# Optimization experiments

Hardware: AMD Instinct MI355X
Metric: run time of the kernel (lower is better)

The kernel has to match this reference:

```python
import jax, jax.numpy as jnp
import numpy as np

B = 2; NPB = 65536; N = B * NPB      # voxels, equal count per batch (divisible by group size)
C = 128; H = 4; DH = C // H          # model dim, heads, head dim
GS = 4096; T = 64                    # window group size, retention chunk length
SPARSE = (32, 468, 468)              # sparse_shape (z, y, x)
WIN = (13, 13, 32)                   # window_shape (x, y, z)


def _mappings(coords):
    # get_window_coors_shift_v2 (shift=False) + x/y Hilbert-like in-window orders, then sort.
    sz, sy, sx = SPARSE
    wx, wy, wz = WIN
    mx = int(np.ceil(sx / wx) + 1); my = int(np.ceil(sy / wy) + 1); mz = int(np.ceil(sz / wz) + 1)
    per = mx * my * mz
    b = coords[:, 0]; z = coords[:, 1]; y = coords[:, 2]; x = coords[:, 3]
    wcx, wcy, wcz = x // wx, y // wy, z // wz
    cx, cy, cz = x % wx, y % wy, z % wz
    bwx = b * per + wcx * (my * mz) + wcy * mz + wcz
    bwy = b * per + wcy * (mx * mz) + wcx * mz + wcz
    wvol = wx * wy * wz
    vx = bwx * wvol + cx * (wy * wz) + cy * wz + cz
    vy = bwy * wvol + cy * (wx * wz) + cx * wz + cz
    return jnp.argsort(vx), jnp.argsort(vy)


def _retnet_block(x, Wq, Wk, Wv, Wg, Wo):
    # x: [G, L, C]; per-head decayed linear attention (RetNet), chunked recurrent form.
    G, L, _ = x.shape
    nch = L // T
    gamma = 1.0 - jnp.exp2(-5.0 - jnp.arange(H, dtype=x.dtype))  # [H]

    def heads(w):
        return (x @ w).reshape(G, L, H, DH).transpose(0, 2, 1, 3)  # [G,H,L,dh]

    q = heads(Wq) * (DH ** -0.5); k = heads(Wk); v = heads(Wv)

    def chunks(t):
        return t.reshape(G, H, nch, T, DH).transpose(2, 0, 1, 3, 4)  # [nch,G,H,T,dh]

    qc, kc, vc = chunks(q), chunks(k), chunks(v)
    i = jnp.arange(T)
    expo = i[:, None] - i[None, :]
    D = jnp.where(expo >= 0, gamma[:, None, None] ** jnp.maximum(expo, 0), 0.0)  # [H,T,T] causal decay
    cross_d = gamma[:, None] ** (i + 1)[None, :]        # [H,T] state->token decay
    kv_d = gamma[:, None] ** (T - 1 - i)[None, :]       # [H,T] token->state decay
    chunk_d = gamma ** T

    def step(S, qkv):  # S: [G,H,dh,dh]
        qt, kt, vt = qkv
        attn = jnp.einsum('ghtd,ghsd->ghts', qt, kt) * D[None]
        inner = jnp.einsum('ghts,ghsd->ghtd', attn, vt)
        cross = jnp.einsum('ghtd,ghde->ghte', qt * cross_d[None, :, :, None], S)
        S = chunk_d[None, :, None, None] * S + jnp.einsum('ghtd,ghte->ghde', kt * kv_d[None, :, :, None], vt)
        return S, inner + cross

    S0 = jnp.zeros((G, H, DH, DH), x.dtype)
    _, ys = jax.lax.scan(step, S0, (qc, kc, vc))  # [nch,G,H,T,dh]
    y = ys.transpose(1, 2, 0, 3, 4).reshape(G, H, L, DH).transpose(0, 2, 1, 3).reshape(G, L, C)
    return x + (y * jax.nn.silu(x @ Wg)) @ Wo


def setup_inputs():
    key = jax.random.key(0)
    ks = jax.random.split(key, 16)
    feats = jax.random.normal(ks[0], (N, C), jnp.float32)
    b = jnp.repeat(jnp.arange(B, dtype=jnp.int32), NPB)
    z = jax.random.randint(ks[1], (N,), 0, SPARSE[0], dtype=jnp.int32)
    y = jax.random.randint(ks[2], (N,), 0, SPARSE[1], dtype=jnp.int32)
    x = jax.random.randint(ks[3], (N,), 0, SPARSE[2], dtype=jnp.int32)
    coords = jnp.stack([b, z, y, x], axis=1)
    w = lambda k: jax.random.normal(k, (C, C), jnp.float32) * (C ** -0.5)
    names = ['Wq0', 'Wk0', 'Wv0', 'Wg0', 'Wo0', 'Wq1', 'Wk1', 'Wv1', 'Wg1', 'Wo1']
    d = {'feats': feats, 'coords': coords}
    for n_, k_ in zip(names, ks[4:14]):
        d[n_] = w(k_)
    return d


def reference(feats, coords, Wq0, Wk0, Wv0, Wg0, Wo0, Wq1, Wk1, Wv1, Wg1, Wo1):
    # Per-batch counts are equal and divisible by GS, so flat2win/win2flat are identity maps.
    ix, iy = _mappings(coords)
    f = feats
    for idx, W in ((ix, (Wq0, Wk0, Wv0, Wg0, Wo0)), (iy, (Wq1, Wk1, Wv1, Wg1, Wo1))):
        xf = f[idx].reshape(-1, GS, C)     # gather sorted windows
        xf = _retnet_block(xf, *W)         # per-window linear RNN
        f = f.at[idx].set(xf.reshape(-1, C))  # scatter back
    return f
```

## Files before the change

### kernel.cpp

```cpp
#include <hip/hip_runtime.h>
#include <hip/hip_bf16.h>

#define NPTS 131072
#define CF   128
#define GS   4096
#define PER  2738
#define NBKT 5476
#define NCHUNK 2048

typedef short v8s __attribute__((ext_vector_type(8)));
typedef float v4f __attribute__((ext_vector_type(4)));
#define MFMA16(a,b,c) __builtin_amdgcn_mfma_f32_16x16x32_bf16(a,b,c,0,0,0)

__device__ __forceinline__ unsigned short f2b(float x) {
    unsigned u = __float_as_uint(x);
    unsigned r = (u + 0x7FFFu + ((u >> 16) & 1u)) >> 16;
    return (unsigned short)r;
}
__device__ __forceinline__ unsigned pack2(float a, float b) {
    return (unsigned)f2b(a) | ((unsigned)f2b(b) << 16);
}
__device__ __forceinline__ float b2f(unsigned short s) {
    return __uint_as_float((unsigned)s << 16);
}

__global__ void k_zero(int* a, int* b, int* c, int* d) {
    int t = blockIdx.x * 256 + threadIdx.x;
    if (t < 8192) { a[t] = 0; b[t] = 0; c[t] = 0; d[t] = 0; }
}

__global__ void k_keys(const int* __restrict__ coords, int* cntx, int* cnty) {
    int j = blockIdx.x * 256 + threadIdx.x;
    if (j >= NPTS) return;
    int b = coords[4*j], z = coords[4*j+1], y = coords[4*j+2], x = coords[4*j+3];
    int wcx = x / 13, wcy = y / 13, wcz = z / 32;
    atomicAdd(&cntx[b * PER + wcx * 74 + wcy * 2 + wcz], 1);
    atomicAdd(&cnty[b * PER + wcy * 74 + wcx * 2 + wcz], 1);
}

__global__ __launch_bounds__(256) void k_bscan(const int* __restrict__ cntx, int* offx,
                                               const int* __restrict__ cnty, int* offy) {
    const int* cnt = blockIdx.x ? cnty : cntx;
    int* off = blockIdx.x ? offy : offx;
    __shared__ int part[256];
    int t = threadIdx.x;
    const int CH = (NBKT + 255) / 256;
    int s = 0;
    for (int i = 0; i < CH; i++) { int idx = t * CH + i; if (idx < NBKT) s += cnt[idx]; }
    part[t] = s;
    __syncthreads();
    for (int d = 1; d < 256; d <<= 1) {
        int v = (t >= d) ? part[t - d] : 0;
        __syncthreads();
        part[t] += v;
        __syncthreads();
    }
    int base = (t == 0) ? 0 : part[t - 1];
    for (int i = 0; i < CH; i++) {
        int idx = t * CH + i;
        if (idx < NBKT) { off[idx] = base; base += cnt[idx]; }
    }
}

__global__ void k_scatter(const int* __restrict__ coords,
                          const int* __restrict__ offx, int* curx, int* bkx,
                          const int* __restrict__ offy, int* cury, int* bky) {
    int j = blockIdx.x * 256 + threadIdx.x;
    if (j >= NPTS) return;
    int b = coords[4*j], z = coords[4*j+1], y = coords[4*j+2], x = coords[4*j+3];
    int wcx = x / 13, wcy = y / 13, wcz = z / 32;
    int cx = x - wcx * 13, cy = y - wcy * 13, cz = z - wcz * 32;
    int px = offx[b*PER + wcx*74 + wcy*2 + wcz] + atomicAdd(&curx[b*PER + wcx*74 + wcy*2 + wcz], 1);
    bkx[px] = ((cx * 416 + cy * 32 + cz) << 17) | j;
    int py = offy[b*PER + wcy*74 + wcx*2 + wcz] + atomicAdd(&cury[b*PER + wcy*74 + wcx*2 + wcz], 1);
    bky[py] = ((cy * 416 + cx * 32 + cz) << 17) | j;
}

__global__ __launch_bounds__(256) void k_bsort(const int* offx, const int* cntx, const int* bkx, int* ix,
                                               const int* offy, const int* cnty, const int* bky, int* iy) {
    const int* off; const int* cnt; const int* bk; int* oidx;
    if (blockIdx.y == 0) { off = offx; cnt = cntx; bk = bkx; oidx = ix; }
    else                 { off = offy; cnt = cnty; bk = bky; oidx = iy; }
    int b = blockIdx.x;
    int n = cnt[b];
    if (n <= 0) return;
    int base = off[b];
    __shared__ int keys[256];
    int t = threadIdx.x;
    if (t < n) keys[t] = bk[base + t];
    __syncthreads();
    if (t < n) {
        int kv = keys[t];
        int r = 0;
        for (int j = 0; j < n; j++) r += (keys[j] < kv);
        oidx[base + r] = kv & 0x1FFFF;
    }
}

struct WP { const float* p[10]; };
__global__ void k_cvtw(WP wp, unsigned short* __restrict__ WT) {
    int i = blockIdx.x * 256 + threadIdx.x;
    int w = i >> 14, r = i & 16383, c = r >> 7, d = r & 127;
    float v = wp.p[w][c * 128 + d];
    if (w == 0 || w == 5) v *= 0.17677669529663687f;
    WT[(size_t)w * 16384 + d * 128 + c] = f2b(v);
}

__global__ __launch_bounds__(256) void k_qkvA(const float* __restrict__ src,
        const int* __restrict__ idx,
        const unsigned short* __restrict__ WTq, const unsigned short* __restrict__ WTk,
        const unsigned short* __restrict__ WTv,
        unsigned short* __restrict__ qb, unsigned short* __restrict__ kb,
        unsigned short* __restrict__ vtb, float* __restrict__ At) {
    __shared__ unsigned short kt[128 * 72];
    __shared__ unsigned short vt[128 * 72];
    const int chunk = blockIdx.x;
    const int t = threadIdx.x, w = t >> 6, lane = t & 63, l15 = lane & 15, kg = lane >> 4;
    const int rtok = chunk * 64 + w * 16 + l15;
    const int srow = idx[rtok];
    const int sloc = w * 16 + l15;
    float w63[4];
#pragma unroll
    for (int h = 0; h < 4; h++) {
        float l2g = log2f(1.f - exp2f(-5.f - (float)h));
        w63[h] = exp2f((float)(63 - sloc) * l2g);
    }
    v8s xf[4];
    const float* xr = src + (size_t)srow * 128;
#pragma unroll
    for (int ks = 0; ks < 4; ks++) {
        int c0 = ks * 32 + kg * 8;
        float4 a = *(const float4*)(xr + c0);
        float4 b = *(const float4*)(xr + c0 + 4);
        v8s v;
        v[0]=(short)f2b(a.x); v[1]=(short)f2b(a.y); v[2]=(short)f2b(a.z); v[3]=(short)f2b(a.w);
        v[4]=(short)f2b(b.x); v[5]=(short)f2b(b.y); v[6]=(short)f2b(b.z); v[7]=(short)f2b(b.w);
        xf[ks] = v;
    }
#pragma unroll
    for (int dt = 0; dt < 8; dt++) {
        v4f acc = {0.f, 0.f, 0.f, 0.f};
#pragma unroll
        for (int ks = 0; ks < 4; ks++) {
            v8s wf = *(const v8s*)(WTq + (size_t)(dt * 16 + l15) * 128 + ks * 32 + kg * 8);
            acc = MFMA16(wf, xf[ks], acc);
        }
        int2 p; p.x = pack2(acc[0], acc[1]); p.y = pack2(acc[2], acc[3]);
        *(int2*)(qb + (size_t)rtok * 128 + dt * 16 + kg * 4) = p;
    }
#pragma unroll
    for (int dt = 0; dt < 8; dt++) {
        v4f acc = {0.f, 0.f, 0.f, 0.f};
#pragma unroll
        for (int ks = 0; ks < 4; ks++) {
            v8s wf = *(const v8s*)(WTk + (size_t)(dt * 16 + l15) * 128 + ks * 32 + kg * 8);
            acc = MFMA16(wf, xf[ks], acc);
        }
        int2 p; p.x = pack2(acc[0], acc[1]); p.y = pack2(acc[2], acc[3]);
        *(int2*)(kb + (size_t)rtok * 128 + dt * 16 + kg * 4) = p;
        float dec = w63[dt >> 1];
        int d0 = dt * 16 + kg * 4;
#pragma unroll
        for (int j = 0; j < 4; j++) kt[(d0 + j) * 72 + sloc] = f2b(acc[j] * dec);
    }
#pragma unroll
    for (int et = 0; et < 8; et++) {
        v4f acc = {0.f, 0.f, 0.f, 0.f};
#pragma unroll
        for (int ks = 0; ks < 4; ks++) {
            v8s wf = *(const v8s*)(WTv + (size_t)(et * 16 + l15) * 128 + ks * 32 + kg * 8);
            acc = MFMA16(xf[ks], wf, acc);
        }
        int e_glob = et * 16 + l15, h = e_glob >> 5, e = e_glob & 31, s0 = w * 16 + kg * 4;
        int2 p; p.x = pack2(acc[0], acc[1]); p.y = pack2(acc[2], acc[3]);
        *(int2*)(vtb + ((size_t)(chunk * 4 + h) * 2048) + e * 64 + s0) = p;
        *(int2*)(vt + e_glob * 72 + s0) = p;
    }
    __syncthreads();
    {
        int h = w, g = chunk >> 6, c = chunk & 63;
        size_t base = ((size_t)(g * 4 + h) * 64 + c) * 1024;
#pragma unroll
        for (int dt2 = 0; dt2 < 2; dt2++)
#pragma unroll
        for (int et2 = 0; et2 < 2; et2++) {
            v4f acc = {0.f, 0.f, 0.f, 0.f};
#pragma unroll
            for (int ks2 = 0; ks2 < 2; ks2++) {
                v8s af = *(const v8s*)(kt + (h * 32 + dt2 * 16 + l15) * 72 + ks2 * 32 + kg * 8);
                v8s bf = *(const v8s*)(vt + (h * 32 + et2 * 16 + l15) * 72 + ks2 * 32 + kg * 8);
                acc = MFMA16(af, bf, acc);
            }
            *(v4f*)(At + base + (et2 * 16 + l15) * 32 + dt2 * 16 + kg * 4) = acc;
        }
    }
}

__global__ __launch_bounds__(256) void k_sscan(const float* __restrict__ At,
                                               unsigned short* __restrict__ Sbt) {
    int b = blockIdx.x, gh = b >> 2, q = b & 3, h = gh & 3;
    int p = q * 256 + threadIdx.x;
    float gT = exp2f(64.f * log2f(1.f - exp2f(-5.f - (float)h)));
    size_t base = (size_t)gh * 64 * 1024 + p;
    float s = 0.f;
#pragma unroll 4
    for (int c = 0; c < 64; c++) {
        float a = At[base + (size_t)c * 1024];
        Sbt[base + (size_t)c * 1024] = f2b(s);
        s = gT * s + a;
    }
}

__global__ __launch_bounds__(256) void k_attnf(const float* __restrict__ src,
        const int* __restrict__ idx,
        const unsigned short* __restrict__ qb, const unsigned short* __restrict__ kb,
        const unsigned short* __restrict__ vtb, const unsigned short* __restrict__ Sbt,
        const unsigned short* __restrict__ WTg, const unsigned short* __restrict__ WTo,
        float* __restrict__ outp) {
    __shared__ float gp[4][144];
    __shared__ unsigned short Pl[64 * 104];
    __shared__ unsigned short VTl[32 * 104];
    __shared__ unsigned short Zl[64 * 136];
    const int chunk = blockIdx.x;
    const int t = threadIdx.x, w = t >> 6, lane = t & 63, l15 = lane & 15, kg = lane >> 4;
    const int rl = w * 16 + l15;
    const int rtok = chunk * 64 + rl;
    const int srow = idx[rtok];
    {
        float l2gv[4];
#pragma unroll
        for (int h = 0; h < 4; h++) l2gv[h] = log2f(1.f - exp2f(-5.f - (float)h));
        for (int i = t; i < 576; i += 256) {
            int h = i / 144, m = i - h * 144;
            gp[h][m] = exp2f((float)(m - 64) * l2gv[h]);
        }
    }
    v4f yacc[8];
#pragma unroll
    for (int i = 0; i < 8; i++) yacc[i] = (v4f){0.f, 0.f, 0.f, 0.f};

    const size_t sb_base = ((size_t)((chunk >> 6) * 4) * 64 + (chunk & 63)) * 1024;
#pragma unroll
    for (int h = 0; h < 4; h++) {
        __syncthreads();
        {
            int e = t >> 3, s0 = (t & 7) * 8;
            v8s vv = *(const v8s*)(vtb + (size_t)(chunk * 4 + h) * 2048 + e * 64 + s0);
            *(v8s*)(VTl + e * 104 + s0) = vv;
            if (t < 128) {
                int e2 = t >> 2, d0 = (t & 3) * 8;
                v8s sv = *(const v8s*)(Sbt + sb_base + (size_t)h * 64 * 1024 + e2 * 32 + d0);
                *(v8s*)(VTl + e2 * 104 + 64 + d0) = sv;
            }
        }
        __syncthreads();
        v8s qf = *(const v8s*)(qb + (size_t)rtok * 128 + h * 32 + kg * 8);
        v4f Tf[4];
#pragma unroll
        for (int st = 0; st < 4; st++) {
            v8s kf = *(const v8s*)(kb + (size_t)(chunk * 64 + st * 16 + l15) * 128 + h * 32 + kg * 8);
            Tf[st] = MFMA16(kf, qf, ((v4f){0.f, 0.f, 0.f, 0.f}));
        }
        float gi1 = gp[h][63], gi2 = gp[h][62], gi3 = gp[h][61];
#pragma unroll
        for (int st = 0; st < 4; st++) {
            int s0 = st * 16 + kg * 4;
            float g0 = gp[h][64 + rl - s0];
            float v0 = (rl >= s0    ) ? Tf[st][0] * g0       : 0.f;
            float v1 = (rl >= s0 + 1) ? Tf[st][1] * g0 * gi1 : 0.f;
            float v2 = (rl >= s0 + 2) ? Tf[st][2] * g0 * gi2 : 0.f;
            float v3 = (rl >= s0 + 3) ? Tf[st][3] * g0 * gi3 : 0.f;
            int2 p; p.x = pack2(v0, v1); p.y = pack2(v2, v3);
            *(int2*)(Pl + rl * 104 + s0) = p;
        }
        {
            float gc = gp[h][65 + rl];
            float q0 = b2f((unsigned short)qf[0]) * gc, q1 = b2f((unsigned short)qf[1]) * gc;
            float q2 = b2f((unsigned short)qf[2]) * gc, q3 = b2f((unsigned short)qf[3]) * gc;
            float q4 = b2f((unsigned short)qf[4]) * gc, q5 = b2f((unsigned short)qf[5]) * gc;
            float q6 = b2f((unsigned short)qf[6]) * gc, q7 = b2f((unsigned short)qf[7]) * gc;
            int2 pa; pa.x = pack2(q0, q1); pa.y = pack2(q2, q3);
            *(int2*)(Pl + rl * 104 + 64 + kg * 8) = pa;
            int2 pb; pb.x = pack2(q4, q5); pb.y = pack2(q6, q7);
            *(int2*)(Pl + rl * 104 + 64 + kg * 8 + 4) = pb;
        }
#pragma unroll
        for (int et = 0; et < 2; et++) {
            v4f acc = yacc[h * 2 + et];
#pragma unroll
            for (int ks = 0; ks < 3; ks++) {
                v8s vf = *(const v8s*)(VTl + (et * 16 + l15) * 104 + ks * 32 + kg * 8);
                v8s pf = *(const v8s*)(Pl + rl * 104 + ks * 32 + kg * 8);
                acc = MFMA16(vf, pf, acc);
            }
            yacc[h * 2 + et] = acc;
        }
    }
    v8s xg[4];
    {
        const float* xr = src + (size_t)srow * 128;
#pragma unroll
        for (int ks = 0; ks < 4; ks++) {
            int c0 = ks * 32 + kg * 8;
            float4 a = *(const float4*)(xr + c0);
            float4 b = *(const float4*)(xr + c0 + 4);
            v8s v;
            v[0]=(short)f2b(a.x); v[1]=(short)f2b(a.y); v[2]=(short)f2b(a.z); v[3]=(short)f2b(a.w);
            v[4]=(short)f2b(b.x); v[5]=(short)f2b(b.y); v[6]=(short)f2b(b.z); v[7]=(short)f2b(b.w);
            xg[ks] = v;
        }
    }
#pragma unroll
    for (int ct = 0; ct < 8; ct++) {
        v4f g = {0.f, 0.f, 0.f, 0.f};
#pragma unroll
        for (int ks = 0; ks < 4; ks++) {
            v8s wf = *(const v8s*)(WTg + (size_t)(ct * 16 + l15) * 128 + ks * 32 + kg * 8);
            g = MFMA16(wf, xg[ks], g);
        }
        v4f yv = yacc[ct];
        float z0 = yv[0] * (g[0] / (1.f + __expf(-g[0])));
        float z1 = yv[1] * (g[1] / (1.f + __expf(-g[1])));
        float z2 = yv[2] * (g[2] / (1.f + __expf(-g[2])));
        float z3 = yv[3] * (g[3] / (1.f + __expf(-g[3])));
        int2 p; p.x = pack2(z0, z1); p.y = pack2(z2, z3);
        *(int2*)(Zl + rl * 136 + ct * 16 + kg * 4) = p;
    }
    v8s zf[4];
#pragma unroll
    for (int ks = 0; ks < 4; ks++)
        zf[ks] = *(const v8s*)(Zl + rl * 136 + ks * 32 + kg * 8);
    const float* xr = src + (size_t)srow * 128;
#pragma unroll
    for (int cot = 0; cot < 8; cot++) {
        v4f acc = {0.f, 0.f, 0.f, 0.f};
#pragma unroll
        for (int ks = 0; ks < 4; ks++) {
            v8s wf = *(const v8s*)(WTo + (size_t)(cot * 16 + l15) * 128 + ks * 32 + kg * 8);
            acc = MFMA16(wf, zf[ks], acc);
        }
        int c0 = cot * 16 + kg * 4;
        float4 xres = *(const float4*)(xr + c0);
        float4 o;
        o.x = xres.x + acc[0]; o.y = xres.y + acc[1];
        o.z = xres.z + acc[2]; o.w = xres.w + acc[3];
        *(float4*)(outp + (size_t)srow * 128 + c0) = o;
    }
}

static void run_pass(const float* src, const int* idx, const unsigned short* WT, int wbase,
                     unsigned short* qb, unsigned short* kb, unsigned short* vtb,
                     float* At, unsigned short* Sbt, float* out, hipStream_t stream) {
    k_qkvA<<<NCHUNK, 256, 0, stream>>>(src, idx, WT + (size_t)(wbase+0)*16384,
                                       WT + (size_t)(wbase+1)*16384, WT + (size_t)(wbase+2)*16384,
                                       qb, kb, vtb, At);
    k_sscan<<<512, 256, 0, stream>>>(At, Sbt);
    k_attnf<<<NCHUNK, 256, 0, stream>>>(src, idx, qb, kb, vtb, Sbt,
                                        WT + (size_t)(wbase+3)*16384, WT + (size_t)(wbase+4)*16384, out);
}

extern "C" void kernel_launch(void* const* d_in, const int* in_sizes, int n_in,
                              void* d_out, int out_size, void* d_ws, size_t ws_size,
                              hipStream_t stream) {
    const float* feats  = (const float*)d_in[0];
    const int*   coords = (const int*)d_in[1];
    float* out = (float*)d_out;

    char* wptr = (char*)d_ws;
    unsigned short* qb  = (unsigned short*)wptr; wptr += (size_t)NPTS * 128 * 2;
    unsigned short* kb  = (unsigned short*)wptr; wptr += (size_t)NPTS * 128 * 2;
    unsigned short* vtb = (unsigned short*)wptr; wptr += (size_t)NPTS * 128 * 2;
    float* At           = (float*)wptr;          wptr += (size_t)NCHUNK * 4096 * 4;
    unsigned short* Sbt = (unsigned short*)wptr; wptr += (size_t)NCHUNK * 4096 * 2;
    unsigned short* WT  = (unsigned short*)wptr; wptr += (size_t)10 * 16384 * 2;
    int* ix   = (int*)wptr; wptr += (size_t)NPTS * 4;
    int* iy   = (int*)wptr; wptr += (size_t)NPTS * 4;
    int* bkx  = (int*)wptr; wptr += (size_t)NPTS * 4;
    int* bky  = (int*)wptr; wptr += (size_t)NPTS * 4;
    int* cntx = (int*)wptr; wptr += 8192 * 4;
    int* cnty = (int*)wptr; wptr += 8192 * 4;
    int* offx = (int*)wptr; wptr += 8192 * 4;
    int* offy = (int*)wptr; wptr += 8192 * 4;
    int* curx = (int*)wptr; wptr += 8192 * 4;
    int* cury = (int*)wptr; wptr += 8192 * 4;

    WP wp;
    for (int i = 0; i < 10; i++) wp.p[i] = (const float*)d_in[2 + i];
    k_cvtw<<<640, 256, 0, stream>>>(wp, WT);

    k_zero<<<32, 256, 0, stream>>>(cntx, cnty, curx, cury);
    k_keys<<<(NPTS + 255) / 256, 256, 0, stream>>>(coords, cntx, cnty);
    k_bscan<<<2, 256, 0, stream>>>(cntx, offx, cnty, offy);
    k_scatter<<<(NPTS + 255) / 256, 256, 0, stream>>>(coords, offx, curx, bkx, offy, cury, bky);
    k_bsort<<<dim3(NBKT, 2), 256, 0, stream>>>(offx, cntx, bkx, ix, offy, cnty, bky, iy);

    run_pass(feats, ix, WT, 0, qb, kb, vtb, At, Sbt, out, stream);
    run_pass(out,   iy, WT, 5, qb, kb, vtb, At, Sbt, out, stream);
}
```

Baseline: 648.3 us.

## Split chunk-state kernel, store decayed K, and replace LDS staging with cross-lane shuffles

The QKV kernel now stages the gathered input rows through shared memory with coalesced loads, and it stores K already scaled by its in-chunk decay. Computing the chunk K^T V state moves into a separate kernel that reads K and V back from global memory. The attention kernel drops its shared-memory buffers and barriers: decay factors are computed in closed form and the P/Z operand layouts are rebuilt with wave shuffles. The state scan preloads all 64 chunk values into registers. This trades an extra launch and extra global traffic for fewer LDS round trips and syncs.

```diff
diff --git a/kernel.cpp b/kernel.cpp
--- a/kernel.cpp
+++ b/kernel.cpp
@@ -2,8 +2,6 @@
 #include <hip/hip_bf16.h>
 
 #define NPTS 131072
-#define CF   128
-#define GS   4096
 #define PER  2738
 #define NBKT 5476
 #define NCHUNK 2048
@@ -22,6 +20,23 @@
 }
 __device__ __forceinline__ float b2f(unsigned short s) {
     return __uint_as_float((unsigned)s << 16);
+}
+
+__device__ __forceinline__ v8s redist(int2 a, int2 b, int lane) {
+    int l15 = lane & 15, kg = lane >> 4;
+    int m0 = l15 + 16 * ((2 * kg) & 3);
+    int m1 = l15 + 16 * ((2 * kg + 1) & 3);
+    int ax0 = __shfl(a.x, m0, 64), ay0 = __shfl(a.y, m0, 64);
+    int ax1 = __shfl(a.x, m1, 64), ay1 = __shfl(a.y, m1, 64);
+    int bx0 = __shfl(b.x, m0, 64), by0 = __shfl(b.y, m0, 64);
+    int bx1 = __shfl(b.x, m1, 64), by1 = __shfl(b.y, m1, 64);
+    bool hi = kg >= 2;
+    union { int i[4]; v8s v; } u;
+    u.i[0] = hi ? bx0 : ax0;
+    u.i[1] = hi ? by0 : ay0;
+    u.i[2] = hi ? bx1 : ax1;
+    u.i[3] = hi ? by1 : ay1;
+    return u.v;
 }
 
 __global__ void k_zero(int* a, int* b, int* c, int* d) {
@@ -106,37 +121,37 @@
     WT[(size_t)w * 16384 + d * 128 + c] = f2b(v);
 }
 
-__global__ __launch_bounds__(256) void k_qkvA(const float* __restrict__ src,
+__global__ __launch_bounds__(256) void k_qkv(const float* __restrict__ src,
         const int* __restrict__ idx,
         const unsigned short* __restrict__ WTq, const unsigned short* __restrict__ WTk,
         const unsigned short* __restrict__ WTv,
-        unsigned short* __restrict__ qb, unsigned short* __restrict__ kb,
-        unsigned short* __restrict__ vtb, float* __restrict__ At) {
-    __shared__ unsigned short kt[128 * 72];
-    __shared__ unsigned short vt[128 * 72];
+        unsigned short* __restrict__ qb, unsigned short* __restrict__ kbh,
+        unsigned short* __restrict__ vtb) {
+    __shared__ unsigned short Xl[64 * 136];
     const int chunk = blockIdx.x;
     const int t = threadIdx.x, w = t >> 6, lane = t & 63, l15 = lane & 15, kg = lane >> 4;
-    const int rtok = chunk * 64 + w * 16 + l15;
-    const int srow = idx[rtok];
+#pragma unroll
+    for (int i = 0; i < 8; i++) {
+        int r = i * 8 + (t >> 5);
+        int col = (t & 31) * 4;
+        int srow = idx[chunk * 64 + r];
+        float4 v = *(const float4*)(src + (size_t)srow * 128 + col);
+        uint2 p; p.x = pack2(v.x, v.y); p.y = pack2(v.z, v.w);
+        *(uint2*)(Xl + r * 136 + col) = p;
+    }
+    __syncthreads();
     const int sloc = w * 16 + l15;
+    const int rtok = chunk * 64 + sloc;
+    v8s xf[4];
+#pragma unroll
+    for (int ks = 0; ks < 4; ks++)
+        xf[ks] = *(const v8s*)(Xl + sloc * 136 + ks * 32 + kg * 8);
     float w63[4];
 #pragma unroll
     for (int h = 0; h < 4; h++) {
         float l2g = log2f(1.f - exp2f(-5.f - (float)h));
         w63[h] = exp2f((float)(63 - sloc) * l2g);
     }
-    v8s xf[4];
-    const float* xr = src + (size_t)srow * 128;
-#pragma unroll
-    for (int ks = 0; ks < 4; ks++) {
-        int c0 = ks * 32 + kg * 8;
-        float4 a = *(const float4*)(xr + c0);
-        float4 b = *(const float4*)(xr + c0 + 4);
-        v8s v;
-        v[0]=(short)f2b(a.x); v[1]=(short)f2b(a.y); v[2]=(short)f2b(a.z); v[3]=(short)f2b(a.w);
-        v[4]=(short)f2b(b.x); v[5]=(short)f2b(b.y); v[6]=(short)f2b(b.z); v[7]=(short)f2b(b.w);
-        xf[ks] = v;
-    }
 #pragma unroll
     for (int dt = 0; dt < 8; dt++) {
         v4f acc = {0.f, 0.f, 0.f, 0.f};
@@ -156,12 +171,9 @@
             v8s wf = *(const v8s*)(WTk + (size_t)(dt * 16 + l15) * 128 + ks * 32 + kg * 8);
             acc = MFMA16(wf, xf[ks], acc);
         }
-        int2 p; p.x = pack2(acc[0], acc[1]); p.y = pack2(acc[2], acc[3]);
-        *(int2*)(kb + (size_t)rtok * 128 + dt * 16 + kg * 4) = p;
         float dec = w63[dt >> 1];
-        int d0 = dt * 16 + kg * 4;
-#pragma unroll
-        for (int j = 0; j < 4; j++) kt[(d0 + j) * 72 + sloc] = f2b(acc[j] * dec);
+        int2 p; p.x = pack2(acc[0] * dec, acc[1] * dec); p.y = pack2(acc[2] * dec, acc[3] * dec);
+        *(int2*)(kbh + (size_t)rtok * 128 + dt * 16 + kg * 4) = p;
     }
 #pragma unroll
     for (int et = 0; et < 8; et++) {
@@ -174,25 +186,38 @@
         int e_glob = et * 16 + l15, h = e_glob >> 5, e = e_glob & 31, s0 = w * 16 + kg * 4;
         int2 p; p.x = pack2(acc[0], acc[1]); p.y = pack2(acc[2], acc[3]);
         *(int2*)(vtb + ((size_t)(chunk * 4 + h) * 2048) + e * 64 + s0) = p;
-        *(int2*)(vt + e_glob * 72 + s0) = p;
+    }
+}
+
+__global__ __launch_bounds__(256) void k_chA(const unsigned short* __restrict__ kbh,
+                                             const unsigned short* __restrict__ vtb,
+                                             float* __restrict__ At) {
+    __shared__ unsigned short kt[128 * 72];
+    const int chunk = blockIdx.x;
+    const int t = threadIdx.x, w = t >> 6, lane = t & 63, l15 = lane & 15, kg = lane >> 4;
+#pragma unroll
+    for (int i = 0; i < 4; i++) {
+        int linear = i * 256 + t;
+        int s = linear >> 4, cs = linear & 15;
+        v8s kv = *(const v8s*)(kbh + (size_t)(chunk * 64 + s) * 128 + cs * 8);
+#pragma unroll
+        for (int j = 0; j < 8; j++) kt[(cs * 8 + j) * 72 + s] = (unsigned short)kv[j];
     }
     __syncthreads();
-    {
-        int h = w, g = chunk >> 6, c = chunk & 63;
-        size_t base = ((size_t)(g * 4 + h) * 64 + c) * 1024;
-#pragma unroll
-        for (int dt2 = 0; dt2 < 2; dt2++)
-#pragma unroll
-        for (int et2 = 0; et2 < 2; et2++) {
-            v4f acc = {0.f, 0.f, 0.f, 0.f};
-#pragma unroll
-            for (int ks2 = 0; ks2 < 2; ks2++) {
-                v8s af = *(const v8s*)(kt + (h * 32 + dt2 * 16 + l15) * 72 + ks2 * 32 + kg * 8);
-                v8s bf = *(const v8s*)(vt + (h * 32 + et2 * 16 + l15) * 72 + ks2 * 32 + kg * 8);
-                acc = MFMA16(af, bf, acc);
-            }
-            *(v4f*)(At + base + (et2 * 16 + l15) * 32 + dt2 * 16 + kg * 4) = acc;
-        }
+    const int h = w, g = chunk >> 6, c = chunk & 63;
+    size_t base = ((size_t)(g * 4 + h) * 64 + c) * 1024;
+#pragma unroll
+    for (int dt2 = 0; dt2 < 2; dt2++)
+#pragma unroll
+    for (int et2 = 0; et2 < 2; et2++) {
+        v4f acc = {0.f, 0.f, 0.f, 0.f};
+#pragma unroll
+        for (int ks2 = 0; ks2 < 2; ks2++) {
+            v8s af = *(const v8s*)(kt + (h * 32 + dt2 * 16 + l15) * 72 + ks2 * 32 + kg * 8);
+            v8s bf = *(const v8s*)(vtb + (size_t)(chunk * 4 + h) * 2048 + (et2 * 16 + l15) * 64 + ks2 * 32 + kg * 8);
+            acc = MFMA16(af, bf, acc);
+        }
+        *(v4f*)(At + base + (et2 * 16 + l15) * 32 + dt2 * 16 + kg * 4) = acc;
     }
 }
 
@@ -201,115 +226,86 @@
     int b = blockIdx.x, gh = b >> 2, q = b & 3, h = gh & 3;
     int p = q * 256 + threadIdx.x;
     float gT = exp2f(64.f * log2f(1.f - exp2f(-5.f - (float)h)));
-    size_t base = (size_t)gh * 64 * 1024 + p;
+    size_t base = (size_t)gh * 65536 + p;
+    float a[64];
+#pragma unroll
+    for (int c = 0; c < 64; c++) a[c] = At[base + (size_t)c * 1024];
     float s = 0.f;
-#pragma unroll 4
+#pragma unroll
     for (int c = 0; c < 64; c++) {
-        float a = At[base + (size_t)c * 1024];
         Sbt[base + (size_t)c * 1024] = f2b(s);
-        s = gT * s + a;
+        s = gT * s + a[c];
     }
 }
 
 __global__ __launch_bounds__(256) void k_attnf(const float* __restrict__ src,
         const int* __restrict__ idx,
-        const unsigned short* __restrict__ qb, const unsigned short* __restrict__ kb,
+        const unsigned short* __restrict__ qb, const unsigned short* __restrict__ kbh,
         const unsigned short* __restrict__ vtb, const unsigned short* __restrict__ Sbt,
         const unsigned short* __restrict__ WTg, const unsigned short* __restrict__ WTo,
         float* __restrict__ outp) {
-    __shared__ float gp[4][144];
-    __shared__ unsigned short Pl[64 * 104];
-    __shared__ unsigned short VTl[32 * 104];
-    __shared__ unsigned short Zl[64 * 136];
     const int chunk = blockIdx.x;
     const int t = threadIdx.x, w = t >> 6, lane = t & 63, l15 = lane & 15, kg = lane >> 4;
     const int rl = w * 16 + l15;
     const int rtok = chunk * 64 + rl;
-    const int srow = idx[rtok];
-    {
-        float l2gv[4];
-#pragma unroll
-        for (int h = 0; h < 4; h++) l2gv[h] = log2f(1.f - exp2f(-5.f - (float)h));
-        for (int i = t; i < 576; i += 256) {
-            int h = i / 144, m = i - h * 144;
-            gp[h][m] = exp2f((float)(m - 64) * l2gv[h]);
-        }
-    }
+    float l2g[4];
+#pragma unroll
+    for (int h = 0; h < 4; h++) l2g[h] = log2f(1.f - exp2f(-5.f - (float)h));
     v4f yacc[8];
 #pragma unroll
     for (int i = 0; i < 8; i++) yacc[i] = (v4f){0.f, 0.f, 0.f, 0.f};
-
-    const size_t sb_base = ((size_t)((chunk >> 6) * 4) * 64 + (chunk & 63)) * 1024;
+    const size_t sb = ((size_t)(chunk >> 6) * 256 + (chunk & 63)) * 1024;
 #pragma unroll
     for (int h = 0; h < 4; h++) {
-        __syncthreads();
-        {
-            int e = t >> 3, s0 = (t & 7) * 8;
-            v8s vv = *(const v8s*)(vtb + (size_t)(chunk * 4 + h) * 2048 + e * 64 + s0);
-            *(v8s*)(VTl + e * 104 + s0) = vv;
-            if (t < 128) {
-                int e2 = t >> 2, d0 = (t & 3) * 8;
-                v8s sv = *(const v8s*)(Sbt + sb_base + (size_t)h * 64 * 1024 + e2 * 32 + d0);
-                *(v8s*)(VTl + e2 * 104 + 64 + d0) = sv;
-            }
-        }
-        __syncthreads();
+        float grow = exp2f((float)(rl - 63) * l2g[h]);
+        float gc   = exp2f((float)(rl + 1)  * l2g[h]);
         v8s qf = *(const v8s*)(qb + (size_t)rtok * 128 + h * 32 + kg * 8);
-        v4f Tf[4];
+        int2 pp[4];
 #pragma unroll
         for (int st = 0; st < 4; st++) {
-            v8s kf = *(const v8s*)(kb + (size_t)(chunk * 64 + st * 16 + l15) * 128 + h * 32 + kg * 8);
-            Tf[st] = MFMA16(kf, qf, ((v4f){0.f, 0.f, 0.f, 0.f}));
-        }
-        float gi1 = gp[h][63], gi2 = gp[h][62], gi3 = gp[h][61];
-#pragma unroll
-        for (int st = 0; st < 4; st++) {
+            v8s kf = *(const v8s*)(kbh + (size_t)(chunk * 64 + st * 16 + l15) * 128 + h * 32 + kg * 8);
+            v4f Tf = MFMA16(kf, qf, ((v4f){0.f, 0.f, 0.f, 0.f}));
             int s0 = st * 16 + kg * 4;
-            float g0 = gp[h][64 + rl - s0];
-            float v0 = (rl >= s0    ) ? Tf[st][0] * g0       : 0.f;
-            float v1 = (rl >= s0 + 1) ? Tf[st][1] * g0 * gi1 : 0.f;
-            float v2 = (rl >= s0 + 2) ? Tf[st][2] * g0 * gi2 : 0.f;
-            float v3 = (rl >= s0 + 3) ? Tf[st][3] * g0 * gi3 : 0.f;
-            int2 p; p.x = pack2(v0, v1); p.y = pack2(v2, v3);
-            *(int2*)(Pl + rl * 104 + s0) = p;
-        }
-        {
-            float gc = gp[h][65 + rl];
-            float q0 = b2f((unsigned short)qf[0]) * gc, q1 = b2f((unsigned short)qf[1]) * gc;
-            float q2 = b2f((unsigned short)qf[2]) * gc, q3 = b2f((unsigned short)qf[3]) * gc;
-            float q4 = b2f((unsigned short)qf[4]) * gc, q5 = b2f((unsigned short)qf[5]) * gc;
-            float q6 = b2f((unsigned short)qf[6]) * gc, q7 = b2f((unsigned short)qf[7]) * gc;
-            int2 pa; pa.x = pack2(q0, q1); pa.y = pack2(q2, q3);
-            *(int2*)(Pl + rl * 104 + 64 + kg * 8) = pa;
-            int2 pb; pb.x = pack2(q4, q5); pb.y = pack2(q6, q7);
-            *(int2*)(Pl + rl * 104 + 64 + kg * 8 + 4) = pb;
-        }
+            float v0 = (rl >= s0    ) ? Tf[0] * grow : 0.f;
+            float v1 = (rl >= s0 + 1) ? Tf[1] * grow : 0.f;
+            float v2 = (rl >= s0 + 2) ? Tf[2] * grow : 0.f;
+            float v3 = (rl >= s0 + 3) ? Tf[3] * grow : 0.f;
+            pp[st].x = pack2(v0, v1); pp[st].y = pack2(v2, v3);
+        }
+        union { int i[4]; v8s v; } pe;
+        pe.i[0] = pack2(b2f((unsigned short)qf[0]) * gc, b2f((unsigned short)qf[1]) * gc);
+        pe.i[1] = pack2(b2f((unsigned short)qf[2]) * gc, b2f((unsigned short)qf[3]) * gc);
+        pe.i[2] = pack2(b2f((unsigned short)qf[4]) * gc, b2f((unsigned short)qf[5]) * gc);
+        pe.i[3] = pack2(b2f((unsigned short)qf[6]) * gc, b2f((unsigned short)qf[7]) * gc);
+        v8s pf0 = redist(pp[0], pp[1], lane);
+        v8s pf1 = redist(pp[2], pp[3], lane);
 #pragma unroll
         for (int et = 0; et < 2; et++) {
             v4f acc = yacc[h * 2 + et];
-#pragma unroll
-            for (int ks = 0; ks < 3; ks++) {
-                v8s vf = *(const v8s*)(VTl + (et * 16 + l15) * 104 + ks * 32 + kg * 8);
-                v8s pf = *(const v8s*)(Pl + rl * 104 + ks * 32 + kg * 8);
-                acc = MFMA16(vf, pf, acc);
-            }
+            size_t vbase = (size_t)(chunk * 4 + h) * 2048 + (et * 16 + l15) * 64;
+            v8s vf0 = *(const v8s*)(vtb + vbase + kg * 8);
+            v8s vf1 = *(const v8s*)(vtb + vbase + 32 + kg * 8);
+            acc = MFMA16(vf0, pf0, acc);
+            acc = MFMA16(vf1, pf1, acc);
+            v8s sf = *(const v8s*)(Sbt + sb + (size_t)h * 65536 + (et * 16 + l15) * 32 + kg * 8);
+            acc = MFMA16(sf, pe.v, acc);
             yacc[h * 2 + et] = acc;
         }
     }
+    const int srow = idx[rtok];
+    const float* xr = src + (size_t)srow * 128;
     v8s xg[4];
-    {
-        const float* xr = src + (size_t)srow * 128;
-#pragma unroll
-        for (int ks = 0; ks < 4; ks++) {
-            int c0 = ks * 32 + kg * 8;
-            float4 a = *(const float4*)(xr + c0);
-            float4 b = *(const float4*)(xr + c0 + 4);
-            v8s v;
-            v[0]=(short)f2b(a.x); v[1]=(short)f2b(a.y); v[2]=(short)f2b(a.z); v[3]=(short)f2b(a.w);
-            v[4]=(short)f2b(b.x); v[5]=(short)f2b(b.y); v[6]=(short)f2b(b.z); v[7]=(short)f2b(b.w);
-            xg[ks] = v;
-        }
-    }
+#pragma unroll
+    for (int ks = 0; ks < 4; ks++) {
+        int c0 = ks * 32 + kg * 8;
+        float4 a = *(const float4*)(xr + c0);
+        float4 b = *(const float4*)(xr + c0 + 4);
+        union { int i[4]; v8s v; } u;
+        u.i[0] = pack2(a.x, a.y); u.i[1] = pack2(a.z, a.w);
+        u.i[2] = pack2(b.x, b.y); u.i[3] = pack2(b.z, b.w);
+        xg[ks] = u.v;
+    }
+    int2 zp[8];
 #pragma unroll
     for (int ct = 0; ct < 8; ct++) {
         v4f g = {0.f, 0.f, 0.f, 0.f};
@@ -323,14 +319,11 @@
         float z1 = yv[1] * (g[1] / (1.f + __expf(-g[1])));
         float z2 = yv[2] * (g[2] / (1.f + __expf(-g[2])));
         float z3 = yv[3] * (g[3] / (1.f + __expf(-g[3])));
-        int2 p; p.x = pack2(z0, z1); p.y = pack2(z2, z3);
-        *(int2*)(Zl + rl * 136 + ct * 16 + kg * 4) = p;
+        zp[ct].x = pack2(z0, z1); zp[ct].y = pack2(z2, z3);
     }
     v8s zf[4];
 #pragma unroll
-    for (int ks = 0; ks < 4; ks++)
-        zf[ks] = *(const v8s*)(Zl + rl * 136 + ks * 32 + kg * 8);
-    const float* xr = src + (size_t)srow * 128;
+    for (int ks = 0; ks < 4; ks++) zf[ks] = redist(zp[2 * ks], zp[2 * ks + 1], lane);
 #pragma unroll
     for (int cot = 0; cot < 8; cot++) {
         v4f acc = {0.f, 0.f, 0.f, 0.f};
@@ -349,13 +342,14 @@
 }
 
 static void run_pass(const float* src, const int* idx, const unsigned short* WT, int wbase,
-                     unsigned short* qb, unsigned short* kb, unsigned short* vtb,
+                     unsigned short* qb, unsigned short* kbh, unsigned short* vtb,
                      float* At, unsigned short* Sbt, float* out, hipStream_t stream) {
-    k_qkvA<<<NCHUNK, 256, 0, stream>>>(src, idx, WT + (size_t)(wbase+0)*16384,
-                                       WT + (size_t)(wbase+1)*16384, WT + (size_t)(wbase+2)*16384,
-                                       qb, kb, vtb, At);
+    k_qkv<<<NCHUNK, 256, 0, stream>>>(src, idx, WT + (size_t)(wbase+0)*16384,
+                                      WT + (size_t)(wbase+1)*16384, WT + (size_t)(wbase+2)*16384,
+                                      qb, kbh, vtb);
+    k_chA<<<NCHUNK, 256, 0, stream>>>(kbh, vtb, At);
     k_sscan<<<512, 256, 0, stream>>>(At, Sbt);
-    k_attnf<<<NCHUNK, 256, 0, stream>>>(src, idx, qb, kb, vtb, Sbt,
+    k_attnf<<<NCHUNK, 256, 0, stream>>>(src, idx, qb, kbh, vtb, Sbt,
                                         WT + (size_t)(wbase+3)*16384, WT + (size_t)(wbase+4)*16384, out);
 }
 
@@ -368,7 +362,7 @@
 
     char* wptr = (char*)d_ws;
     unsigned short* qb  = (unsigned short*)wptr; wptr += (size_t)NPTS * 128 * 2;
-    unsigned short* kb  = (unsigned short*)wptr; wptr += (size_t)NPTS * 128 * 2;
+    unsigned short* kbh = (unsigned short*)wptr; wptr += (size_t)NPTS * 128 * 2;
     unsigned short* vtb = (unsigned short*)wptr; wptr += (size_t)NPTS * 128 * 2;
     float* At           = (float*)wptr;          wptr += (size_t)NCHUNK * 4096 * 4;
     unsigned short* Sbt = (unsigned short*)wptr; wptr += (size_t)NCHUNK * 4096 * 2;
@@ -394,6 +388,6 @@
     k_scatter<<<(NPTS + 255) / 256, 256, 0, stream>>>(coords, offx, curx, bkx, offy, cury, bky);
     k_bsort<<<dim3(NBKT, 2), 256, 0, stream>>>(offx, cntx, bkx, ix, offy, cnty, bky, iy);
 
-    run_pass(feats, ix, WT, 0, qb, kb, vtb, At, Sbt, out, stream);
-    run_pass(out,   iy, WT, 5, qb, kb, vtb, At, Sbt, out, stream);
-}
+    run_pass(feats, ix, WT, 0, qb, kbh, vtb, At, Sbt, out, stream);
+    run_pass(out,   iy, WT, 5, qb, kbh, vtb, At, Sbt, out, stream);
+}
```

After: 670.6 us. 3.4% more time.
